# Kernel optimization log

Hardware: AMD Instinct MI355X
Metric: run time of the kernel (lower is better)

## Reference

```python
import jax, jax.numpy as jnp
import numpy as np

B, A, D = 16384, 50, 256
ALPHA = 0.2  # LeakyReLU negative slope


def setup_inputs() -> dict:
    key = jax.random.key(0)
    k1, k2, k3 = jax.random.split(key, 3)
    attrs_emb = jax.random.normal(k1, (B, A, D), dtype=jnp.float32)
    entity_emb = jax.random.normal(k2, (B, D), dtype=jnp.float32)
    # xavier_uniform on (2D, 1) with gain 1.414
    limit = 1.414 * np.sqrt(6.0 / (2 * D + 1))
    a = jax.random.uniform(k3, (2 * D, 1), dtype=jnp.float32, minval=-limit, maxval=limit)
    return {"attrs_emb": attrs_emb, "entity_emb": entity_emb, "a": a}


def reference(attrs_emb, entity_emb, a):
    d = attrs_emb.shape[-1]
    attr_num = attrs_emb.shape[1]
    a_attr = a[:d, 0]     # (D,)
    a_ent = a[d:, 0]      # (D,)
    # concat([attrs, entity], -1) @ a == attrs @ a_attr + entity @ a_ent (split dot, same math)
    e = jnp.einsum('bad,d->ba', attrs_emb, a_attr) + (entity_emb @ a_ent)[:, None]  # (B, A)
    e = jax.nn.leaky_relu(e, negative_slope=ALPHA)
    attention = jax.nn.softmax(e, axis=1) * attr_num  # (B, A)
    out = jnp.einsum('ba,bad->bd', attention, attrs_emb)  # (B, D)
    return out
```

## Files before the change

### kernel.cpp

```cpp
#include <hip/hip_runtime.h>
#include <math.h>


#define BN 16384
#define AN 50
#define DN 256
#define ALPHA 0.2f

__global__ __launch_bounds__(256) void struct_attn_kernel(
    const float* __restrict__ attrs,
    const float* __restrict__ ent,
    const float* __restrict__ avec,
    float* __restrict__ out) {
  const int b = blockIdx.x;
  const int t = threadIdx.x;
  const int w = t >> 6;
  const int lane = t & 63;

  __shared__ float e_buf[AN];
  __shared__ float att_buf[AN];
  __shared__ float ent_buf[4];
  __shared__ __align__(16) float pbuf[4][DN];

  const float4* attrs4 = reinterpret_cast<const float4*>(attrs) + (size_t)b * (AN * DN / 4);
  const float4 aa = reinterpret_cast<const float4*>(avec)[lane];

  float4 v[13];
  float p[13];
#pragma unroll
  for (int i = 0; i < 13; ++i) {
    if (i < 12 || w < 2) {
      v[i] = attrs4[i * 256 + t];
      p[i] = v[i].x * aa.x + v[i].y * aa.y + v[i].z * aa.z + v[i].w * aa.w;
    } else {
      p[i] = 0.f;
    }
  }

#pragma unroll
  for (int i = 0; i < 13; ++i) {
    float s = p[i];
    s += __shfl_xor(s, 1);
    s += __shfl_xor(s, 2);
    s += __shfl_xor(s, 4);
    s += __shfl_xor(s, 8);
    s += __shfl_xor(s, 16);
    s += __shfl_xor(s, 32);
    p[i] = s;
  }
  if (lane == 0) {
#pragma unroll
    for (int i = 0; i < 13; ++i) {
      if (i < 12 || w < 2) e_buf[4 * i + w] = p[i];
    }
  }

  {
    float q = ent[(size_t)b * DN + t] * avec[DN + t];
    q += __shfl_xor(q, 1);
    q += __shfl_xor(q, 2);
    q += __shfl_xor(q, 4);
    q += __shfl_xor(q, 8);
    q += __shfl_xor(q, 16);
    q += __shfl_xor(q, 32);
    if (lane == 0) ent_buf[w] = q;
  }
  __syncthreads();

  if (w == 0) {
    float entd = ent_buf[0] + ent_buf[1] + ent_buf[2] + ent_buf[3];
    float el = (lane < AN) ? (e_buf[lane] + entd) : -INFINITY;
    el = (el > 0.f) ? el : ALPHA * el;
    float m = el;
    m = fmaxf(m, __shfl_xor(m, 1));
    m = fmaxf(m, __shfl_xor(m, 2));
    m = fmaxf(m, __shfl_xor(m, 4));
    m = fmaxf(m, __shfl_xor(m, 8));
    m = fmaxf(m, __shfl_xor(m, 16));
    m = fmaxf(m, __shfl_xor(m, 32));
    float pe = (lane < AN) ? __expf(el - m) : 0.f;
    float s = pe;
    s += __shfl_xor(s, 1);
    s += __shfl_xor(s, 2);
    s += __shfl_xor(s, 4);
    s += __shfl_xor(s, 8);
    s += __shfl_xor(s, 16);
    s += __shfl_xor(s, 32);
    if (lane < AN) att_buf[lane] = pe * ((float)AN / s);
  }
  __syncthreads();

  float4 o = make_float4(0.f, 0.f, 0.f, 0.f);
#pragma unroll
  for (int i = 0; i < 13; ++i) {
    if (i < 12 || w < 2) {
      float at = att_buf[4 * i + w];
      o.x += at * v[i].x;
      o.y += at * v[i].y;
      o.z += at * v[i].z;
      o.w += at * v[i].w;
    }
  }
  reinterpret_cast<float4*>(&pbuf[w][0])[lane] = o;
  __syncthreads();

  float r = pbuf[0][t] + pbuf[1][t] + pbuf[2][t] + pbuf[3][t];
  out[(size_t)b * DN + t] = r;
}

extern "C" void kernel_launch(void* const* d_in, const int* in_sizes, int n_in,
                              void* d_out, int out_size, void* d_ws, size_t ws_size,
                              hipStream_t stream) {
  const float* attrs = (const float*)d_in[0];
  const float* ent   = (const float*)d_in[1];
  const float* avec  = (const float*)d_in[2];
  float* out = (float*)d_out;
  struct_attn_kernel<<<BN, 256, 0, stream>>>(attrs, ent, avec, out);
}
```

Measured before the change: 1.052 ms.

## Process eight rows per block with double-buffered register prefetch of attributes

Each block now handles eight batch rows instead of one and keeps two register sets of attribute tiles. It loads the next row while computing the current one, to hide global-memory latency in a kernel that loads everything once. Every wave now computes the softmax redundantly and broadcasts weights with lane shuffles, which removes one barrier and the attention buffer in shared memory. A custom barrier waits only on LDS counters, so outstanding global prefetches are not drained at each sync. The cost is higher register pressure and eight times fewer blocks in the grid.

```diff
diff --git a/kernel.cpp b/kernel.cpp
--- a/kernel.cpp
+++ b/kernel.cpp
@@ -6,47 +6,46 @@
 #define AN 50
 #define DN 256
 #define ALPHA 0.2f
+#define RPB 8
 
-__global__ __launch_bounds__(256) void struct_attn_kernel(
-    const float* __restrict__ attrs,
-    const float* __restrict__ ent,
-    const float* __restrict__ avec,
-    float* __restrict__ out) {
-  const int b = blockIdx.x;
-  const int t = threadIdx.x;
-  const int w = t >> 6;
-  const int lane = t & 63;
+__device__ __forceinline__ float wave_sum(float x) {
+  x += __shfl_xor(x, 1);
+  x += __shfl_xor(x, 2);
+  x += __shfl_xor(x, 4);
+  x += __shfl_xor(x, 8);
+  x += __shfl_xor(x, 16);
+  x += __shfl_xor(x, 32);
+  return x;
+}
 
-  __shared__ float e_buf[AN];
-  __shared__ float att_buf[AN];
-  __shared__ float ent_buf[4];
-  __shared__ __align__(16) float pbuf[4][DN];
+__device__ __forceinline__ float wave_max(float x) {
+  x = fmaxf(x, __shfl_xor(x, 1));
+  x = fmaxf(x, __shfl_xor(x, 2));
+  x = fmaxf(x, __shfl_xor(x, 4));
+  x = fmaxf(x, __shfl_xor(x, 8));
+  x = fmaxf(x, __shfl_xor(x, 16));
+  x = fmaxf(x, __shfl_xor(x, 32));
+  return x;
+}
 
-  const float4* attrs4 = reinterpret_cast<const float4*>(attrs) + (size_t)b * (AN * DN / 4);
-  const float4 aa = reinterpret_cast<const float4*>(avec)[lane];
+#define BARRIER()                                        \
+  do {                                                   \
+    asm volatile("s_waitcnt lgkmcnt(0)" ::: "memory");   \
+    __builtin_amdgcn_s_barrier();                        \
+    asm volatile("" ::: "memory");                       \
+  } while (0)
 
-  float4 v[13];
+__device__ __forceinline__ void process_row(
+    const float4 (&v)[13], int bb, int t, int w, int lane, const float4& aa,
+    float aent, const float* __restrict__ ent, float* __restrict__ out,
+    float* e_buf, float* ent_s, float (*pbuf)[DN]) {
   float p[13];
 #pragma unroll
   for (int i = 0; i < 13; ++i) {
     if (i < 12 || w < 2) {
-      v[i] = attrs4[i * 256 + t];
       p[i] = v[i].x * aa.x + v[i].y * aa.y + v[i].z * aa.z + v[i].w * aa.w;
-    } else {
-      p[i] = 0.f;
+      p[i] = wave_sum(p[i]);
     }
-  }
-
-#pragma unroll
-  for (int i = 0; i < 13; ++i) {
-    float s = p[i];
-    s += __shfl_xor(s, 1);
-    s += __shfl_xor(s, 2);
-    s += __shfl_xor(s, 4);
-    s += __shfl_xor(s, 8);
-    s += __shfl_xor(s, 16);
-    s += __shfl_xor(s, 32);
-    p[i] = s;
   }
   if (lane == 0) {
 #pragma unroll
@@ -54,47 +53,26 @@
       if (i < 12 || w < 2) e_buf[4 * i + w] = p[i];
     }
   }
+  {
+    float q = ent[(size_t)bb * DN + t] * aent;
+    q = wave_sum(q);
+    if (lane == 0) ent_s[w] = q;
+  }
+  BARRIER();
 
-  {
-    float q = ent[(size_t)b * DN + t] * avec[DN + t];
-    q += __shfl_xor(q, 1);
-    q += __shfl_xor(q, 2);
-    q += __shfl_xor(q, 4);
-    q += __shfl_xor(q, 8);
-    q += __shfl_xor(q, 16);
-    q += __shfl_xor(q, 32);
-    if (lane == 0) ent_buf[w] = q;
-  }
-  __syncthreads();
-
-  if (w == 0) {
-    float entd = ent_buf[0] + ent_buf[1] + ent_buf[2] + ent_buf[3];
-    float el = (lane < AN) ? (e_buf[lane] + entd) : -INFINITY;
-    el = (el > 0.f) ? el : ALPHA * el;
-    float m = el;
-    m = fmaxf(m, __shfl_xor(m, 1));
-    m = fmaxf(m, __shfl_xor(m, 2));
-    m = fmaxf(m, __shfl_xor(m, 4));
-    m = fmaxf(m, __shfl_xor(m, 8));
-    m = fmaxf(m, __shfl_xor(m, 16));
-    m = fmaxf(m, __shfl_xor(m, 32));
-    float pe = (lane < AN) ? __expf(el - m) : 0.f;
-    float s = pe;
-    s += __shfl_xor(s, 1);
-    s += __shfl_xor(s, 2);
-    s += __shfl_xor(s, 4);
-    s += __shfl_xor(s, 8);
-    s += __shfl_xor(s, 16);
-    s += __shfl_xor(s, 32);
-    if (lane < AN) att_buf[lane] = pe * ((float)AN / s);
-  }
-  __syncthreads();
+  float entd = ent_s[0] + ent_s[1] + ent_s[2] + ent_s[3];
+  float el = (lane < AN) ? (e_buf[lane] + entd) : -1e30f;
+  el = (el > 0.f) ? el : ALPHA * el;
+  float m = wave_max(el);
+  float pe = (lane < AN) ? __expf(el - m) : 0.f;
+  float s = wave_sum(pe);
+  float att = pe * ((float)AN / s);
 
   float4 o = make_float4(0.f, 0.f, 0.f, 0.f);
 #pragma unroll
   for (int i = 0; i < 13; ++i) {
     if (i < 12 || w < 2) {
-      float at = att_buf[4 * i + w];
+      float at = __shfl(att, 4 * i + w);
       o.x += at * v[i].x;
       o.y += at * v[i].y;
       o.z += at * v[i].z;
@@ -102,10 +80,46 @@
     }
   }
   reinterpret_cast<float4*>(&pbuf[w][0])[lane] = o;
-  __syncthreads();
+  BARRIER();
 
   float r = pbuf[0][t] + pbuf[1][t] + pbuf[2][t] + pbuf[3][t];
-  out[(size_t)b * DN + t] = r;
+  out[(size_t)bb * DN + t] = r;
+}
+
+#define LOAD(vX, bb)                                                   \
+  do {                                                                 \
+    const float4* __restrict__ p4 = attrs4 + (size_t)(bb) * 3200;      \
+    _Pragma("unroll") for (int i = 0; i < 12; ++i) vX[i] =             \
+        p4[i * 256 + t];                                               \
+    if (w < 2) vX[12] = p4[12 * 256 + t];                              \
+  } while (0)
+
+__global__ __launch_bounds__(256) void struct_attn_kernel(
+    const float* __restrict__ attrs, const float* __restrict__ ent,
+    const float* __restrict__ avec, float* __restrict__ out) {
+  const int t = threadIdx.x;
+  const int w = t >> 6;
+  const int lane = t & 63;
+  const int b0 = blockIdx.x * RPB;
+
+  __shared__ float e_buf[AN];
+  __shared__ float ent_s[4];
+  __shared__ __align__(16) float pbuf[4][DN];
+
+  const float4* attrs4 = reinterpret_cast<const float4*>(attrs);
+  const float4 aa = reinterpret_cast<const float4*>(avec)[lane];
+  const float aent = avec[DN + t];
+
+  float4 vA[13], vB[13];
+
+  LOAD(vA, b0);
+#pragma unroll
+  for (int j = 0; j < RPB; j += 2) {
+    LOAD(vB, b0 + j + 1);
+    process_row(vA, b0 + j, t, w, lane, aa, aent, ent, out, e_buf, ent_s, pbuf);
+    if (j + 2 < RPB) LOAD(vA, b0 + j + 2);
+    process_row(vB, b0 + j + 1, t, w, lane, aa, aent, ent, out, e_buf, ent_s, pbuf);
+  }
 }
 
 extern "C" void kernel_launch(void* const* d_in, const int* in_sizes, int n_in,
@@ -115,5 +129,5 @@
   const float* ent   = (const float*)d_in[1];
   const float* avec  = (const float*)d_in[2];
   float* out = (float*)d_out;
-  struct_attn_kernel<<<BN, 256, 0, stream>>>(attrs, ent, avec, out);
+  struct_attn_kernel<<<BN / RPB, 256, 0, stream>>>(attrs, ent, avec, out);
 }
```

New measurement: 1.067 ms. About the same (+1.4%).
